# Kernel tuning notes

Measured on AMD Instinct MI355X. Metric: run time of the kernel, lower is better.

The kernel has to match this reference:

```python
import jax, jax.numpy as jnp
import numpy as np

EPS = 1e-6
GRID_ORDER_K = 4
DIST_K = 3


def _smallest_k(d, k):
    # k smallest values along last axis, ascending (torch.topk largest=False)
    return -jax.lax.top_k(-d, k)[0]


def _radius_loss(real, fake):
    qs = jnp.array([0.05, 0.1, 0.25, 0.5, 0.75, 0.9, 0.95], jnp.float32)
    fq = jnp.quantile(fake[:, :, 2], qs)
    rq = jnp.quantile(real[:, :, 2], qs)
    return jnp.mean((fq - rq) ** 2)


def _grid_density_loss(real, fake):
    qs = jnp.array([0.05, 0.25, 0.5, 0.75, 0.95], jnp.float32)
    lx = jnp.mean((jnp.quantile(fake[:, :, 0], qs) - jnp.quantile(real[:, :, 0], qs)) ** 2)
    ly = jnp.mean((jnp.quantile(fake[:, :, 1], qs) - jnp.quantile(real[:, :, 1], qs)) ** 2)
    return (lx + ly) / 2


def _knn_dists_flat(x, k):
    # x: [B,N,3]; pairwise dist on xy with +eps under sqrt as in source
    xy = x[:, :, :2]
    d = jnp.sqrt(((xy[:, :, None, :] - xy[:, None, :, :]) ** 2).sum(-1) + EPS)  # [B,N,N]
    d = _smallest_k(d, k)  # [B,N,k]
    return d.reshape(x.shape[0], -1)


def _distance_loss(real, fake):
    qs = jnp.array([0.05, 0.5, 0.95], jnp.float32)
    rq = jnp.quantile(_knn_dists_flat(real, DIST_K), qs, axis=1)  # [3,B]
    fq = jnp.quantile(_knn_dists_flat(fake, DIST_K), qs, axis=1)
    return jnp.mean((fq - rq) ** 2)


def _hexatic_order(coords, k):
    # coords: [B,N,2] -> psi: [B,N] complex
    B, N, _ = coords.shape
    diffs = coords[:, :, None, :] - coords[:, None, :, :]  # [B,N,N,2]
    dx = diffs[..., 0]
    dx = dx + EPS * (jnp.abs(dx) < EPS).astype(dx.dtype)
    angles = jnp.arctan2(diffs[..., 1], dx)
    e_iktheta = jnp.exp(1j * k * angles)  # [B,N,N] complex64
    dist = jnp.sqrt((diffs ** 2).sum(-1) + EPS)
    eye = jnp.eye(N, dtype=bool)[None]
    dist = jnp.where(eye, jnp.inf, dist)
    kth = jax.lax.stop_gradient(_smallest_k(dist, k)[..., -1])  # [B,N]
    sigma = jnp.maximum(0.1 * jnp.maximum(kth[..., None], EPS), EPS)
    arg = jnp.clip((kth[..., None] - dist) / sigma, -50.0, 50.0)
    w = jax.nn.sigmoid(arg)
    psi = (e_iktheta * w).sum(2) / jnp.maximum(w.sum(2), EPS)
    return psi


def _grid_order_loss(samples):
    psi = _hexatic_order(samples[:, :, :2], GRID_ORDER_K)
    return -jnp.mean(jnp.sqrt(psi * jnp.conj(psi))).real


def _physical_feasibility_loss(fake):
    xy = fake[:, :, :2]
    r = fake[:, :, 2]
    N = fake.shape[1]
    sq = ((xy[:, :, None, :] - xy[:, None, :, :]) ** 2).sum(-1)
    d = jnp.sqrt(jnp.where(sq <= 0, 1.0, sq))  # safe sqrt (guard grads at 0)
    d = jnp.where(sq <= 0, 0.0, d)
    tril = jnp.tril(jnp.ones((N, N), bool))[None]
    d = jnp.where(tril, d, 0.0)
    d = jnp.where(d <= 0, jnp.inf, d)
    radii_pair = jnp.abs(r)[:, None, :] + jnp.abs(r)[:, :, None]
    overlap = jax.nn.relu(radii_pair - (d + 1e-4))  # sqrt(x**2)==x for x>=0
    return overlap.sum() / (radii_pair.sum() / 2)


def _gan_loss(fake_outputs):
    t = 0.9  # ones_like - 0.1 label smoothing
    logp = jnp.maximum(jnp.log(fake_outputs), -100.0)
    log1mp = jnp.maximum(jnp.log(1.0 - fake_outputs), -100.0)
    return -jnp.mean(t * logp + (1.0 - t) * log1mp)


def setup_inputs() -> dict:
    key = jax.random.key(0)
    k1, k2, k3 = jax.random.split(key, 3)
    B, N = 4, 2048
    real_images = jax.random.normal(k1, (B, N, 3), jnp.float32)
    fake_images = jax.random.normal(k2, (B, N, 3), jnp.float32)
    fake_outputs = jax.random.uniform(k3, (B, 1), jnp.float32, 1e-3, 1.0 - 1e-3)
    return {"real_images": real_images, "fake_images": fake_images, "fake_outputs": fake_outputs}


def reference(real_images, fake_images, fake_outputs):
    loss = _radius_loss(real_images, fake_images)
    loss = loss + _physical_feasibility_loss(fake_images)
    loss = loss + _gan_loss(fake_outputs)
    loss = loss + _grid_density_loss(real_images, fake_images)
    loss = loss + _distance_loss(real_images, fake_images)
    loss = loss + _grid_order_loss(fake_images)
    return loss
```

## Files before the change

### kernel.cpp

```cpp
#include <hip/hip_runtime.h>
#include <math.h>

#define B_SZ   4
#define N_PTS  2048
#define EPSF   1e-6f
#define CAP    500

#define WS_KNN_R 0
#define WS_KNN_F 24576
#define WS_FEAS  49152
#define WS_PSIP  50176
#define WS_RSUM  51200
#define WS_Q     51204
#define WS_TICK  51264
#define QZF (WS_Q + 0)
#define QZR (WS_Q + 7)
#define QXF (WS_Q + 14)
#define QXR (WS_Q + 19)
#define QYF (WS_Q + 24)
#define QYR (WS_Q + 29)
#define QDR (WS_Q + 34)
#define QDF (WS_Q + 46)
#define COMP_SCALE 256.0f
#define KNN_SCALE  1024.0f

__constant__ float c_qs7[7] = {0.05f, 0.1f, 0.25f, 0.5f, 0.75f, 0.9f, 0.95f};
__constant__ float c_qs5[5] = {0.05f, 0.25f, 0.5f, 0.75f, 0.95f};
__constant__ float c_qs3[3] = {0.05f, 0.5f, 0.95f};

#define CE(a, b) { float _lo = fminf(a, b), _hi = fmaxf(a, b); a = _lo; b = _hi; }

__device__ __forceinline__ void ins3a(float m[3], float v) {
    float h0 = fmaxf(m[0], v); m[0] = fminf(m[0], v);
    float h1 = fmaxf(m[1], h0); m[1] = fminf(m[1], h0);
    m[2] = fminf(m[2], h1);
}
__device__ __forceinline__ void ins5a(float m[5], float v) {
    float h0 = fmaxf(m[0], v); m[0] = fminf(m[0], v);
    float h1 = fmaxf(m[1], h0); m[1] = fminf(m[1], h0);
    float h2 = fmaxf(m[2], h1); m[2] = fminf(m[2], h1);
    float h3 = fmaxf(m[3], h2); m[3] = fminf(m[3], h2);
    m[4] = fminf(m[4], h3);
}

__global__ __launch_bounds__(256) void hs_pair_kernel(const float* __restrict__ real,
                                                      const float* __restrict__ fake,
                                                      float* __restrict__ ws) {
    __shared__ float2 sxy[N_PTS];
    __shared__ float sr[N_PTS];
    __shared__ unsigned short slist[4 * 2 * CAP];
    __shared__ float s4[4];
    const int tid = threadIdx.x, wave = tid >> 6, lane = tid & 63;
    const int blk = blockIdx.x;
    if (blk == 0 && tid == 0) ((unsigned int*)ws)[WS_TICK] = 0u;

    if (blk < 1024) {
        const int b = blk >> 8, grp = blk & 255;
        const float* src = fake + (size_t)b * N_PTS * 3;
        for (int t = tid; t < N_PTS; t += 256) {
            const float* p = src + t * 3;
            sxy[t] = make_float2(p[0], p[1]);
            sr[t]  = fabsf(p[2]);
        }
        __syncthreads();
        const int p0 = grp * 8 + wave * 2;
        float px[2], py[2], pri[2], m[2][5];
#pragma unroll
        for (int t = 0; t < 2; ++t) {
            px[t] = sxy[p0 + t].x; py[t] = sxy[p0 + t].y;
            pri[t] = sr[p0 + t] - 1e-4f;
            m[t][0] = m[t][1] = m[t][2] = m[t][3] = m[t][4] = INFINITY;
        }
        float acc = 0.f;
        for (int j = lane; j < N_PTS; j += 64) {
            float2 q = sxy[j]; float br = sr[j];
#pragma unroll
            for (int t = 0; t < 2; ++t) {
                float dx = px[t] - q.x, dy = py[t] - q.y;
                float sq = fmaf(dx, dx, dy * dy);
                ins5a(m[t], sq);
                float ov = fmaxf((pri[t] + br) - sqrtf(sq), 0.f);
                acc += (sq > 0.f) ? ov : 0.f;
            }
        }
#pragma unroll
        for (int off = 1; off < 64; off <<= 1) {
#pragma unroll
            for (int t = 0; t < 2; ++t) {
                float b0 = __shfl_xor(m[t][0], off);
                float b1 = __shfl_xor(m[t][1], off);
                float b2 = __shfl_xor(m[t][2], off);
                float b3 = __shfl_xor(m[t][3], off);
                float b4 = __shfl_xor(m[t][4], off);
                float l0 = fminf(m[t][0], b4);
                float l1 = fminf(m[t][1], b3);
                float l2 = fminf(m[t][2], b2);
                float l3 = fminf(m[t][3], b1);
                float l4 = fminf(m[t][4], b0);
                CE(l0, l3); CE(l1, l4); CE(l0, l2); CE(l1, l3);
                CE(l0, l1); CE(l2, l4); CE(l1, l2); CE(l3, l4); CE(l2, l3);
                m[t][0] = l0; m[t][1] = l1; m[t][2] = l2; m[t][3] = l3; m[t][4] = l4;
            }
        }
        if (lane == 0) {
            float* kout = ws + WS_KNN_F + b * (N_PTS * 3);
#pragma unroll
            for (int t = 0; t < 2; ++t) {
                const int i = p0 + t;
                kout[i * 3 + 0] = sqrtf(m[t][0] + EPSF);
                kout[i * 3 + 1] = sqrtf(m[t][1] + EPSF);
                kout[i * 3 + 2] = sqrtf(m[t][2] + EPSF);
            }
        }
        float kth[2], invs[2], T2[2];
#pragma unroll
        for (int t = 0; t < 2; ++t) {
            kth[t] = sqrtf(m[t][4] + EPSF);
            const float sigma = fmaxf(0.1f * fmaxf(kth[t], EPSF), EPSF);
            invs[t] = 1.f / sigma;
            const float T = kth[t] + 50.f * sigma;
            T2[t] = T * T;
        }
        unsigned int cnt[2] = {0u, 0u};
        const int lbase = wave * 2 * CAP;
        for (int it = 0; it < 32; ++it) {
            const int j = it * 64 + lane;
            float2 q = sxy[j];
#pragma unroll
            for (int t = 0; t < 2; ++t) {
                float dx = px[t] - q.x, dy = py[t] - q.y;
                float sq = fmaf(dx, dx, dy * dy);
                const bool p = (sq <= T2[t]);
                const unsigned long long mk = __ballot(p);
                const unsigned int below = __builtin_amdgcn_mbcnt_hi(
                    (unsigned int)(mk >> 32),
                    __builtin_amdgcn_mbcnt_lo((unsigned int)mk, 0u));
                const unsigned int off = cnt[t] + below;
                if (p && off < CAP) slist[lbase + t * CAP + off] = (unsigned short)j;
                cnt[t] += (unsigned int)__popcll((long long)mk);
            }
        }
        float mypsi = 0.f;
#pragma unroll
        for (int t = 0; t < 2; ++t) {
            float swv = 0.f, srev = 0.f, simv = 0.f;
            if (cnt[t] <= CAP) {
                const int len = (int)cnt[t];
                for (int i = lane; i < len; i += 64) {
                    const int j = slist[lbase + t * CAP + i];
                    float2 q = sxy[j];
                    float dx = px[t] - q.x, dy = py[t] - q.y;
                    float sq = fmaf(dx, dx, dy * dy);
                    float dist = sqrtf(sq + EPSF);
                    dist = (j == p0 + t) ? INFINITY : dist;
                    float a = dx + ((fabsf(dx) < EPSF) ? EPSF : 0.f);
                    float arg = fminf(fmaxf((kth[t] - dist) * invs[t], -50.f), 50.f);
                    float e = __expf(-arg);
                    float w = __builtin_amdgcn_rcpf(1.f + e);
                    float aa = a * a, bb = dy * dy;
                    float n2 = aa + bb;
                    float z2r = aa - bb;
                    float t0 = a * dy; float z2i = t0 + t0;
                    float inv = __builtin_amdgcn_rcpf(n2);
                    float ur = z2r * inv, ui = z2i * inv;
                    float e4r = fmaf(ur, ur, -(ui * ui));
                    float t1 = ur * ui; float e4i = t1 + t1;
                    swv += w;
                    srev = fmaf(w, e4r, srev);
                    simv = fmaf(w, e4i, simv);
                }
            } else {
                for (int j = lane; j < N_PTS; j += 64) {
                    float2 q = sxy[j];
                    float dx = px[t] - q.x, dy = py[t] - q.y;
                    float sq = fmaf(dx, dx, dy * dy);
                    float dist = sqrtf(sq + EPSF);
                    dist = (j == p0 + t) ? INFINITY : dist;
                    float a = dx + ((fabsf(dx) < EPSF) ? EPSF : 0.f);
                    float arg = fminf(fmaxf((kth[t] - dist) * invs[t], -50.f), 50.f);
                    float e = __expf(-arg);
                    float w = __builtin_amdgcn_rcpf(1.f + e);
                    float aa = a * a, bb = dy * dy;
                    float n2 = aa + bb;
                    float z2r = aa - bb;
                    float t0 = a * dy; float z2i = t0 + t0;
                    float inv = __builtin_amdgcn_rcpf(n2);
                    float ur = z2r * inv, ui = z2i * inv;
                    float e4r = fmaf(ur, ur, -(ui * ui));
                    float t1 = ur * ui; float e4i = t1 + t1;
                    swv += w;
                    srev = fmaf(w, e4r, srev);
                    simv = fmaf(w, e4i, simv);
                }
            }
#pragma unroll
            for (int off = 1; off < 64; off <<= 1) {
                swv  += __shfl_xor(swv, off);
                srev += __shfl_xor(srev, off);
                simv += __shfl_xor(simv, off);
            }
            if (lane == 0) {
                const float den = fmaxf(swv, EPSF);
                const float pr = srev / den, pi = simv / den;
                mypsi += sqrtf(fmaf(pr, pr, pi * pi));
            }
        }
        float accw = acc;
#pragma unroll
        for (int off = 1; off < 64; off <<= 1) accw += __shfl_xor(accw, off);
        if (lane == 0) s4[wave] = accw;
        __syncthreads();
        if (tid == 0) ws[WS_FEAS + blk] = s4[0] + s4[1] + s4[2] + s4[3];
        __syncthreads();
        if (lane == 0) s4[wave] = mypsi;
        __syncthreads();
        if (tid == 0) ws[WS_PSIP + blk] = s4[0] + s4[1] + s4[2] + s4[3];
        if (grp == 0) {
            float rs = 0.f;
            for (int t = tid; t < N_PTS; t += 256) rs += sr[t];
#pragma unroll
            for (int off = 1; off < 64; off <<= 1) rs += __shfl_xor(rs, off);
            __syncthreads();
            if (lane == 0) s4[wave] = rs;
            __syncthreads();
            if (tid == 0) ws[WS_RSUM + b] = s4[0] + s4[1] + s4[2] + s4[3];
        }
    } else {
        const int rb = blk - 1024;
        const int b = rb >> 7, grp = rb & 127;
        const float* src = real + (size_t)b * N_PTS * 3;
        for (int t = tid; t < N_PTS; t += 256) {
            const float* p = src + t * 3;
            sxy[t] = make_float2(p[0], p[1]);
        }
        __syncthreads();
        const int p0 = grp * 16 + wave * 4;
        float px[4], py[4], m[4][3];
#pragma unroll
        for (int t = 0; t < 4; ++t) {
            px[t] = sxy[p0 + t].x; py[t] = sxy[p0 + t].y;
            m[t][0] = m[t][1] = m[t][2] = INFINITY;
        }
        for (int j = lane; j < N_PTS; j += 64) {
            float2 q = sxy[j];
#pragma unroll
            for (int t = 0; t < 4; ++t) {
                float dx = px[t] - q.x, dy = py[t] - q.y;
                float sq = fmaf(dx, dx, dy * dy);
                ins3a(m[t], sq);
            }
        }
#pragma unroll
        for (int off = 1; off < 64; off <<= 1) {
#pragma unroll
            for (int t = 0; t < 4; ++t) {
                float b0 = __shfl_xor(m[t][0], off);
                float b1 = __shfl_xor(m[t][1], off);
                float b2 = __shfl_xor(m[t][2], off);
                float l0 = fminf(m[t][0], b2);
                float l1 = fminf(m[t][1], b1);
                float l2 = fminf(m[t][2], b0);
                CE(l0, l1); CE(l0, l2); CE(l1, l2);
                m[t][0] = l0; m[t][1] = l1; m[t][2] = l2;
            }
        }
        if (lane == 0) {
            float* kout = ws + WS_KNN_R + b * (N_PTS * 3);
#pragma unroll
            for (int t = 0; t < 4; ++t) {
                const int i = p0 + t;
                kout[i * 3 + 0] = sqrtf(m[t][0] + EPSF);
                kout[i * 3 + 1] = sqrtf(m[t][1] + EPSF);
                kout[i * 3 + 2] = sqrtf(m[t][2] + EPSF);
            }
        }
    }
}

__global__ __launch_bounds__(256) void hs_quant_kernel(const float* __restrict__ real,
                                                       const float* __restrict__ fake,
                                                       const float* __restrict__ fouts,
                                                       float* __restrict__ ws,
                                                       float* __restrict__ out) {
    __shared__ unsigned int hist[4][4096];
    __shared__ unsigned int s_wsum[4];
    __shared__ float sred[256];
    __shared__ int s_last;
    unsigned int* wsu = (unsigned int*)ws;
    const int tid = threadIdx.x, wave = tid >> 6, lane = tid & 63;
    const int aid = blockIdx.x;

    const float* src; int step, n, nq, slot; float vlo, vw; const float* qs;
    if (aid < 6) {
        src = ((aid & 1) ? real : fake) + ((aid < 2) ? 2 : ((aid < 4) ? 0 : 1));
        step = 3; n = 8192;
        nq = (aid < 2) ? 7 : 5;
        slot = (aid < 2) ? (QZF + aid * 7) : (QXF + (aid - 2) * 5);
        vlo = -8.f; vw = 1.f / COMP_SCALE;
        qs = (aid < 2) ? c_qs7 : c_qs5;
    } else {
        const int a = aid - 6;
        src = ws + ((a < 4) ? WS_KNN_R + a * (N_PTS * 3) : WS_KNN_F + (a - 4) * (N_PTS * 3));
        step = 1; n = N_PTS * 3; nq = 3;
        slot = (a < 4) ? (QDR + a * 3) : (QDF + (a - 4) * 3);
        vlo = 0.f; vw = 1.f / KNN_SCALE;
        qs = c_qs3;
    }

    unsigned int* hflat = &hist[0][0];
#pragma unroll
    for (int i = 0; i < 64; ++i) hflat[i * 256 + tid] = 0u;
    __syncthreads();

    const float scale = (aid < 6) ? COMP_SCALE : KNN_SCALE;
    const float bias  = (aid < 6) ? 8.0f : 0.0f;
    for (int e = tid; e < n; e += 256) {
        const float v = src[(size_t)e * step];
        int bin = (int)floorf((v + bias) * scale);
        bin = (bin < 0) ? 0 : (bin > 4095 ? 4095 : bin);
        atomicAdd(&hist[wave][bin], 1u);
    }
    __syncthreads();

    unsigned int c[16], ps = 0;
    const int base = tid * 16;
#pragma unroll
    for (int i = 0; i < 16; ++i) {
        c[i] = hist[0][base + i] + hist[1][base + i] + hist[2][base + i] + hist[3][base + i];
        ps += c[i];
    }
    unsigned int incl = ps;
#pragma unroll
    for (int off = 1; off < 64; off <<= 1) {
        unsigned int nb = (unsigned int)__shfl_up((int)incl, off);
        if (lane >= off) incl += nb;
    }
    if (lane == 63) s_wsum[wave] = incl;
    __syncthreads();
    unsigned int woff = 0;
    for (int w2 = 0; w2 < wave; ++w2) woff += s_wsum[w2];
    unsigned int run = incl - ps + woff;
    unsigned int* sh_cum = &hist[0][0];
#pragma unroll
    for (int i = 0; i < 16; ++i) { run += c[i]; sh_cum[base + i] = run; }
    __syncthreads();

    if (tid < nq) {
        const float pos = qs[tid] * (float)(n - 1);
        const int k = (int)pos;
        const float frac = pos - (float)k;
        float v2[2];
#pragma unroll
        for (int t = 0; t < 2; ++t) {
            const unsigned int r = (unsigned int)(k + t);
            int lo_ = 0, hi_ = 4095;
            while (lo_ < hi_) {
                const int mid = (lo_ + hi_) >> 1;
                if (sh_cum[mid] > r) hi_ = mid; else lo_ = mid + 1;
            }
            const unsigned int excl = (lo_ > 0) ? sh_cum[lo_ - 1] : 0u;
            const unsigned int cnt  = sh_cum[lo_] - excl;
            v2[t] = vlo + ((float)lo_ + ((float)(r - excl) + 0.5f) / (float)cnt) * vw;
        }
        ws[slot + tid] = v2[0] + frac * (v2[1] - v2[0]);
    }

    __threadfence();
    __syncthreads();
    if (tid == 0) {
        const unsigned int t = atomicAdd(&wsu[WS_TICK], 1u);
        s_last = (t == 13u) ? 1 : 0;
    }
    __syncthreads();
    if (!s_last) return;
    __threadfence();

    float fs = 0.f, ps2 = 0.f;
    for (int t = tid; t < 1024; t += 256) {
        fs  += ws[WS_FEAS + t];
        ps2 += ws[WS_PSIP + t];
    }
    sred[tid] = fs;
    __syncthreads();
    for (int s = 128; s > 0; s >>= 1) {
        if (tid < s) sred[tid] += sred[tid + s];
        __syncthreads();
    }
    const float s_feas = sred[0];
    __syncthreads();
    sred[tid] = ps2;
    __syncthreads();
    for (int s = 128; s > 0; s >>= 1) {
        if (tid < s) sred[tid] += sred[tid + s];
        __syncthreads();
    }
    if (tid == 0) {
        const float psi_sum = sred[0];
        const float rsum = ws[WS_RSUM + 0] + ws[WS_RSUM + 1] + ws[WS_RSUM + 2] + ws[WS_RSUM + 3];
        float loss = 0.f;
        float sacc = 0.f;
        for (int qq = 0; qq < 7; ++qq) { float d = ws[QZF + qq] - ws[QZR + qq]; sacc += d * d; }
        loss += sacc / 7.f;
        loss += (0.5f * s_feas) / ((float)N_PTS * rsum);
        float g = 0.f;
        for (int b = 0; b < B_SZ; ++b) {
            float p = fouts[b];
            g += 0.9f * fmaxf(logf(p), -100.f) + 0.1f * fmaxf(logf(1.f - p), -100.f);
        }
        loss += -g / (float)B_SZ;
        float sx = 0.f, sy = 0.f;
        for (int qq = 0; qq < 5; ++qq) {
            float dx = ws[QXF + qq] - ws[QXR + qq]; sx += dx * dx;
            float dy = ws[QYF + qq] - ws[QYR + qq]; sy += dy * dy;
        }
        loss += 0.5f * (sx / 5.f + sy / 5.f);
        float sd = 0.f;
        for (int t = 0; t < 12; ++t) { float d = ws[QDF + t] - ws[QDR + t]; sd += d * d; }
        loss += sd / 12.f;
        loss += -psi_sum / (float)(B_SZ * N_PTS);
        out[0] = loss;
    }
}

extern "C" void kernel_launch(void* const* d_in, const int* in_sizes, int n_in,
                              void* d_out, int out_size, void* d_ws, size_t ws_size,
                              hipStream_t stream) {
    (void)in_sizes; (void)n_in; (void)out_size; (void)ws_size;
    const float* real  = (const float*)d_in[0];
    const float* fake  = (const float*)d_in[1];
    const float* fouts = (const float*)d_in[2];
    float* out = (float*)d_out;
    float* ws  = (float*)d_ws;

    hipLaunchKernelGGL(hs_pair_kernel,  dim3(1536), dim3(256), 0, stream, real, fake, ws);
    hipLaunchKernelGGL(hs_quant_kernel, dim3(14),   dim3(256), 0, stream, real, fake, fouts, ws, out);
}
```

Measured before the change: 111.5 us.

## Move coordinate-quantile histograms into pair kernel and halve histogram bins

The six coordinate quantile histograms (z, x, y for real and fake) move into the first kernel as extra blocks, so they run alongside the pairwise work instead of in the tail quantile kernel. That kernel now handles only the eight kNN-distance histograms. Bin counts drop from 4096 to 2048 by halving the scales, and the kNN histogram adds a two-way replica per wave to reduce atomic contention. The coarser bins make the quantile approximation less precise, and the shared-memory union grows the pair kernel's LDS footprint to the histogram size.

```diff
diff --git a/kernel.cpp b/kernel.cpp
--- a/kernel.cpp
+++ b/kernel.cpp
@@ -21,14 +21,18 @@
 #define QYR (WS_Q + 29)
 #define QDR (WS_Q + 34)
 #define QDF (WS_Q + 46)
-#define COMP_SCALE 256.0f
-#define KNN_SCALE  1024.0f
+#define COMP_SCALE 128.0f
+#define KNN_SCALE  512.0f
 
 __constant__ float c_qs7[7] = {0.05f, 0.1f, 0.25f, 0.5f, 0.75f, 0.9f, 0.95f};
 __constant__ float c_qs5[5] = {0.05f, 0.25f, 0.5f, 0.75f, 0.95f};
 __constant__ float c_qs3[3] = {0.05f, 0.5f, 0.95f};
 
 #define CE(a, b) { float _lo = fminf(a, b), _hi = fmaxf(a, b); a = _lo; b = _hi; }
+
+__device__ __forceinline__ int clamp_bin(int b) {
+    return (b < 0) ? 0 : (b > 2047 ? 2047 : b);
+}
 
 __device__ __forceinline__ void ins3a(float m[3], float v) {
     float h0 = fmaxf(m[0], v); m[0] = fminf(m[0], v);
@@ -43,37 +47,107 @@
     m[4] = fminf(m[4], h3);
 }
 
+union SmemA {
+    struct {
+        float2 sxy[N_PTS];
+        float  sr[N_PTS];
+        unsigned short slist[4 * 2 * CAP];
+    } p;
+    unsigned int hist[4][2048];
+};
+
 __global__ __launch_bounds__(256) void hs_pair_kernel(const float* __restrict__ real,
                                                       const float* __restrict__ fake,
                                                       float* __restrict__ ws) {
-    __shared__ float2 sxy[N_PTS];
-    __shared__ float sr[N_PTS];
-    __shared__ unsigned short slist[4 * 2 * CAP];
+    __shared__ SmemA sm;
     __shared__ float s4[4];
+    __shared__ unsigned int su4[4];
     const int tid = threadIdx.x, wave = tid >> 6, lane = tid & 63;
     const int blk = blockIdx.x;
     if (blk == 0 && tid == 0) ((unsigned int*)ws)[WS_TICK] = 0u;
 
-    if (blk < 1024) {
-        const int b = blk >> 8, grp = blk & 255;
+    if (blk < 6) {
+        const int aid = blk;
+        const float* src = ((aid & 1) ? real : fake) + ((aid < 2) ? 2 : ((aid < 4) ? 0 : 1));
+        const int nq = (aid < 2) ? 7 : 5;
+        const int slot = (aid < 2) ? (QZF + aid * 7) : (QXF + (aid - 2) * 5);
+        const float* qs = (aid < 2) ? c_qs7 : c_qs5;
+
+        unsigned int* hflat = &sm.hist[0][0];
+        for (int i = 0; i < 32; ++i) hflat[i * 256 + tid] = 0u;
+        __syncthreads();
+        for (int u = 0; u < 32; ++u) {
+            const float v = src[(size_t)(u * 256 + tid) * 3];
+            const int bin = clamp_bin((int)floorf((v + 8.0f) * COMP_SCALE));
+            atomicAdd(&sm.hist[wave][bin], 1u);
+        }
+        __syncthreads();
+        unsigned int c[8], ps = 0;
+        const int base = tid * 8;
+#pragma unroll
+        for (int i = 0; i < 8; ++i) {
+            c[i] = sm.hist[0][base + i] + sm.hist[1][base + i]
+                 + sm.hist[2][base + i] + sm.hist[3][base + i];
+            ps += c[i];
+        }
+        unsigned int incl = ps;
+#pragma unroll
+        for (int off = 1; off < 64; off <<= 1) {
+            unsigned int nb = (unsigned int)__shfl_up((int)incl, off);
+            if (lane >= off) incl += nb;
+        }
+        if (lane == 63) su4[wave] = incl;
+        __syncthreads();
+        unsigned int woff = 0;
+        for (int w2 = 0; w2 < wave; ++w2) woff += su4[w2];
+        unsigned int run = incl - ps + woff;
+#pragma unroll
+        for (int i = 0; i < 8; ++i) { run += c[i]; hflat[base + i] = run; }
+        __syncthreads();
+        if (tid < nq) {
+            const float pos = qs[tid] * (float)(8192 - 1);
+            const int k = (int)pos;
+            const float frac = pos - (float)k;
+            float v2[2];
+#pragma unroll
+            for (int t = 0; t < 2; ++t) {
+                const unsigned int r = (unsigned int)(k + t);
+                int lo_ = 0, hi_ = 2047;
+                while (lo_ < hi_) {
+                    const int mid = (lo_ + hi_) >> 1;
+                    if (hflat[mid] > r) hi_ = mid; else lo_ = mid + 1;
+                }
+                const unsigned int excl = (lo_ > 0) ? hflat[lo_ - 1] : 0u;
+                const unsigned int cnt  = hflat[lo_] - excl;
+                const float cden = (cnt > 0u) ? (float)cnt : 1.0f;
+                v2[t] = -8.0f + ((float)lo_ + ((float)(r - excl) + 0.5f) / cden) * (1.0f / COMP_SCALE);
+            }
+            ws[slot + tid] = v2[0] + frac * (v2[1] - v2[0]);
+        }
+        return;
+    }
+
+    if (blk < 1030) {
+        const int fb = blk - 6;
+        const int b = fb >> 8, grp = fb & 255;
         const float* src = fake + (size_t)b * N_PTS * 3;
         for (int t = tid; t < N_PTS; t += 256) {
             const float* p = src + t * 3;
-            sxy[t] = make_float2(p[0], p[1]);
-            sr[t]  = fabsf(p[2]);
+            sm.p.sxy[t] = make_float2(p[0], p[1]);
+            sm.p.sr[t]  = fabsf(p[2]);
         }
         __syncthreads();
         const int p0 = grp * 8 + wave * 2;
         float px[2], py[2], pri[2], m[2][5];
 #pragma unroll
         for (int t = 0; t < 2; ++t) {
-            px[t] = sxy[p0 + t].x; py[t] = sxy[p0 + t].y;
-            pri[t] = sr[p0 + t] - 1e-4f;
+            px[t] = sm.p.sxy[p0 + t].x; py[t] = sm.p.sxy[p0 + t].y;
+            pri[t] = sm.p.sr[p0 + t] - 1e-4f;
             m[t][0] = m[t][1] = m[t][2] = m[t][3] = m[t][4] = INFINITY;
         }
         float acc = 0.f;
         for (int j = lane; j < N_PTS; j += 64) {
-            float2 q = sxy[j]; float br = sr[j];
+            float2 q = sm.p.sxy[j]; float br = sm.p.sr[j];
 #pragma unroll
             for (int t = 0; t < 2; ++t) {
                 float dx = px[t] - q.x, dy = py[t] - q.y;
@@ -125,7 +199,7 @@
         const int lbase = wave * 2 * CAP;
         for (int it = 0; it < 32; ++it) {
             const int j = it * 64 + lane;
-            float2 q = sxy[j];
+            float2 q = sm.p.sxy[j];
 #pragma unroll
             for (int t = 0; t < 2; ++t) {
                 float dx = px[t] - q.x, dy = py[t] - q.y;
@@ -136,7 +210,7 @@
                     (unsigned int)(mk >> 32),
                     __builtin_amdgcn_mbcnt_lo((unsigned int)mk, 0u));
                 const unsigned int off = cnt[t] + below;
-                if (p && off < CAP) slist[lbase + t * CAP + off] = (unsigned short)j;
+                if (p && off < CAP) sm.p.slist[lbase + t * CAP + off] = (unsigned short)j;
                 cnt[t] += (unsigned int)__popcll((long long)mk);
             }
         }
@@ -147,8 +221,8 @@
             if (cnt[t] <= CAP) {
                 const int len = (int)cnt[t];
                 for (int i = lane; i < len; i += 64) {
-                    const int j = slist[lbase + t * CAP + i];
-                    float2 q = sxy[j];
+                    const int j = sm.p.slist[lbase + t * CAP + i];
+                    float2 q = sm.p.sxy[j];
                     float dx = px[t] - q.x, dy = py[t] - q.y;
                     float sq = fmaf(dx, dx, dy * dy);
                     float dist = sqrtf(sq + EPSF);
@@ -171,7 +245,7 @@
                 }
             } else {
                 for (int j = lane; j < N_PTS; j += 64) {
-                    float2 q = sxy[j];
+                    float2 q = sm.p.sxy[j];
                     float dx = px[t] - q.x, dy = py[t] - q.y;
                     float sq = fmaf(dx, dx, dy * dy);
                     float dist = sqrtf(sq + EPSF);
@@ -210,14 +284,14 @@
         for (int off = 1; off < 64; off <<= 1) accw += __shfl_xor(accw, off);
         if (lane == 0) s4[wave] = accw;
         __syncthreads();
-        if (tid == 0) ws[WS_FEAS + blk] = s4[0] + s4[1] + s4[2] + s4[3];
+        if (tid == 0) ws[WS_FEAS + fb] = s4[0] + s4[1] + s4[2] + s4[3];
         __syncthreads();
         if (lane == 0) s4[wave] = mypsi;
         __syncthreads();
-        if (tid == 0) ws[WS_PSIP + blk] = s4[0] + s4[1] + s4[2] + s4[3];
+        if (tid == 0) ws[WS_PSIP + fb] = s4[0] + s4[1] + s4[2] + s4[3];
         if (grp == 0) {
             float rs = 0.f;
-            for (int t = tid; t < N_PTS; t += 256) rs += sr[t];
+            for (int t = tid; t < N_PTS; t += 256) rs += sm.p.sr[t];
 #pragma unroll
             for (int off = 1; off < 64; off <<= 1) rs += __shfl_xor(rs, off);
             __syncthreads();
@@ -226,23 +300,23 @@
             if (tid == 0) ws[WS_RSUM + b] = s4[0] + s4[1] + s4[2] + s4[3];
         }
     } else {
-        const int rb = blk - 1024;
+        const int rb = blk - 1030;
         const int b = rb >> 7, grp = rb & 127;
         const float* src = real + (size_t)b * N_PTS * 3;
         for (int t = tid; t < N_PTS; t += 256) {
             const float* p = src + t * 3;
-            sxy[t] = make_float2(p[0], p[1]);
+            sm.p.sxy[t] = make_float2(p[0], p[1]);
         }
         __syncthreads();
         const int p0 = grp * 16 + wave * 4;
         float px[4], py[4], m[4][3];
 #pragma unroll
         for (int t = 0; t < 4; ++t) {
-            px[t] = sxy[p0 + t].x; py[t] = sxy[p0 + t].y;
+            px[t] = sm.p.sxy[p0 + t].x; py[t] = sm.p.sxy[p0 + t].y;
             m[t][0] = m[t][1] = m[t][2] = INFINITY;
         }
         for (int j = lane; j < N_PTS; j += 64) {
-            float2 q = sxy[j];
+            float2 q = sm.p.sxy[j];
 #pragma unroll
             for (int t = 0; t < 4; ++t) {
                 float dx = px[t] - q.x, dy = py[t] - q.y;
@@ -277,57 +351,43 @@
     }
 }
 
-__global__ __launch_bounds__(256) void hs_quant_kernel(const float* __restrict__ real,
-                                                       const float* __restrict__ fake,
-                                                       const float* __restrict__ fouts,
+__global__ __launch_bounds__(256) void hs_quant_kernel(const float* __restrict__ fouts,
                                                        float* __restrict__ ws,
                                                        float* __restrict__ out) {
-    __shared__ unsigned int hist[4][4096];
+    __shared__ unsigned int hist[4][2048][2];
     __shared__ unsigned int s_wsum[4];
     __shared__ float sred[256];
     __shared__ int s_last;
     unsigned int* wsu = (unsigned int*)ws;
     const int tid = threadIdx.x, wave = tid >> 6, lane = tid & 63;
-    const int aid = blockIdx.x;
-
-    const float* src; int step, n, nq, slot; float vlo, vw; const float* qs;
-    if (aid < 6) {
-        src = ((aid & 1) ? real : fake) + ((aid < 2) ? 2 : ((aid < 4) ? 0 : 1));
-        step = 3; n = 8192;
-        nq = (aid < 2) ? 7 : 5;
-        slot = (aid < 2) ? (QZF + aid * 7) : (QXF + (aid - 2) * 5);
-        vlo = -8.f; vw = 1.f / COMP_SCALE;
-        qs = (aid < 2) ? c_qs7 : c_qs5;
-    } else {
-        const int a = aid - 6;
-        src = ws + ((a < 4) ? WS_KNN_R + a * (N_PTS * 3) : WS_KNN_F + (a - 4) * (N_PTS * 3));
-        step = 1; n = N_PTS * 3; nq = 3;
-        slot = (a < 4) ? (QDR + a * 3) : (QDF + (a - 4) * 3);
-        vlo = 0.f; vw = 1.f / KNN_SCALE;
-        qs = c_qs3;
-    }
-
-    unsigned int* hflat = &hist[0][0];
-#pragma unroll
+    const int a = blockIdx.x;
+
+    const float* src = ws + ((a < 4) ? WS_KNN_R + a * (N_PTS * 3)
+                                     : WS_KNN_F + (a - 4) * (N_PTS * 3));
+    const int n = N_PTS * 3;
+    const int slot = (a < 4) ? (QDR + a * 3) : (QDF + (a - 4) * 3);
+
+    unsigned int* hflat = &hist[0][0][0];
     for (int i = 0; i < 64; ++i) hflat[i * 256 + tid] = 0u;
     __syncthreads();
 
-    const float scale = (aid < 6) ? COMP_SCALE : KNN_SCALE;
-    const float bias  = (aid < 6) ? 8.0f : 0.0f;
-    for (int e = tid; e < n; e += 256) {
-        const float v = src[(size_t)e * step];
-        int bin = (int)floorf((v + bias) * scale);
-        bin = (bin < 0) ? 0 : (bin > 4095 ? 4095 : bin);
-        atomicAdd(&hist[wave][bin], 1u);
-    }
-    __syncthreads();
-
-    unsigned int c[16], ps = 0;
-    const int base = tid * 16;
-#pragma unroll
-    for (int i = 0; i < 16; ++i) {
-        c[i] = hist[0][base + i] + hist[1][base + i] + hist[2][base + i] + hist[3][base + i];
-        ps += c[i];
+    const unsigned int rep = (unsigned int)(lane & 1);
+    for (int u = 0; u < 24; ++u) {
+        const float v = src[u * 256 + tid];
+        const int bin = clamp_bin((int)floorf(v * KNN_SCALE));
+        atomicAdd(&hist[wave][bin][rep], 1u);
+    }
+    __syncthreads();
+
+    unsigned int c[8], ps = 0;
+    const int base = tid * 8;
+#pragma unroll
+    for (int i = 0; i < 8; ++i) {
+        unsigned int s = 0;
+#pragma unroll
+        for (int w = 0; w < 4; ++w)
+            s += hist[w][base + i][0] + hist[w][base + i][1];
+        c[i] = s; ps += s;
     }
     unsigned int incl = ps;
 #pragma unroll
@@ -340,27 +400,27 @@
     unsigned int woff = 0;
     for (int w2 = 0; w2 < wave; ++w2) woff += s_wsum[w2];
     unsigned int run = incl - ps + woff;
-    unsigned int* sh_cum = &hist[0][0];
-#pragma unroll
-    for (int i = 0; i < 16; ++i) { run += c[i]; sh_cum[base + i] = run; }
-    __syncthreads();
-
-    if (tid < nq) {
-        const float pos = qs[tid] * (float)(n - 1);
+#pragma unroll
+    for (int i = 0; i < 8; ++i) { run += c[i]; hflat[base + i] = run; }
+    __syncthreads();
+
+    if (tid < 3) {
+        const float pos = c_qs3[tid] * (float)(n - 1);
         const int k = (int)pos;
         const float frac = pos - (float)k;
         float v2[2];
 #pragma unroll
         for (int t = 0; t < 2; ++t) {
             const unsigned int r = (unsigned int)(k + t);
-            int lo_ = 0, hi_ = 4095;
+            int lo_ = 0, hi_ = 2047;
             while (lo_ < hi_) {
                 const int mid = (lo_ + hi_) >> 1;
-                if (sh_cum[mid] > r) hi_ = mid; else lo_ = mid + 1;
-            }
-            const unsigned int excl = (lo_ > 0) ? sh_cum[lo_ - 1] : 0u;
-            const unsigned int cnt  = sh_cum[lo_] - excl;
-            v2[t] = vlo + ((float)lo_ + ((float)(r - excl) + 0.5f) / (float)cnt) * vw;
+                if (hflat[mid] > r) hi_ = mid; else lo_ = mid + 1;
+            }
+            const unsigned int excl = (lo_ > 0) ? hflat[lo_ - 1] : 0u;
+            const unsigned int cnt  = hflat[lo_] - excl;
+            const float cden = (cnt > 0u) ? (float)cnt : 1.0f;
+            v2[t] = ((float)lo_ + ((float)(r - excl) + 0.5f) / cden) * (1.0f / KNN_SCALE);
         }
         ws[slot + tid] = v2[0] + frac * (v2[1] - v2[0]);
     }
@@ -369,7 +429,7 @@
     __syncthreads();
     if (tid == 0) {
         const unsigned int t = atomicAdd(&wsu[WS_TICK], 1u);
-        s_last = (t == 13u) ? 1 : 0;
+        s_last = (t == 7u) ? 1 : 0;
     }
     __syncthreads();
     if (!s_last) return;
@@ -432,6 +492,6 @@
     float* out = (float*)d_out;
     float* ws  = (float*)d_ws;
 
-    hipLaunchKernelGGL(hs_pair_kernel,  dim3(1536), dim3(256), 0, stream, real, fake, ws);
-    hipLaunchKernelGGL(hs_quant_kernel, dim3(14),   dim3(256), 0, stream, real, fake, fouts, ws, out);
-}
+    hipLaunchKernelGGL(hs_pair_kernel,  dim3(1542), dim3(256), 0, stream, real, fake, ws);
+    hipLaunchKernelGGL(hs_quant_kernel, dim3(8),    dim3(256), 0, stream, fouts, ws, out);
+}
```

Measured after the change: 112.1 us. No clear change (+0.6%).
